# Kernel tuning notes

Measured on AMD Instinct MI355X. Metric: run time of the kernel, lower is better.

The kernel has to match this reference:

```python
import jax, jax.numpy as jnp
import numpy as np

EMBED_DIM = 1024
NUM_HEADS = 16
HEAD_DIM = EMBED_DIM // NUM_HEADS


def setup_inputs() -> dict:
    key = jax.random.key(0)
    ks = jax.random.split(key, 9)
    s = 1.0 / np.sqrt(EMBED_DIM)
    x = jax.random.normal(ks[0], (2, 2048, EMBED_DIM), dtype=jnp.float32)
    # nn.Linear weights are [out, in]; store transposed [in, out] for x @ W
    Wq = jax.random.uniform(ks[1], (EMBED_DIM, EMBED_DIM), jnp.float32, -s, s)
    bq = jax.random.uniform(ks[2], (EMBED_DIM,), jnp.float32, -s, s)
    Wk = jax.random.uniform(ks[3], (EMBED_DIM, EMBED_DIM), jnp.float32, -s, s)
    bk = jax.random.uniform(ks[4], (EMBED_DIM,), jnp.float32, -s, s)
    Wv = jax.random.uniform(ks[5], (EMBED_DIM, EMBED_DIM), jnp.float32, -s, s)
    bv = jax.random.uniform(ks[6], (EMBED_DIM,), jnp.float32, -s, s)
    Wo = jax.random.uniform(ks[7], (EMBED_DIM, EMBED_DIM), jnp.float32, -s, s)
    bo = jax.random.uniform(ks[8], (EMBED_DIM,), jnp.float32, -s, s)
    return {"x": x, "Wq": Wq, "bq": bq, "Wk": Wk, "bk": bk,
            "Wv": Wv, "bv": bv, "Wo": Wo, "bo": bo}


def reference(x, Wq, bq, Wk, bk, Wv, bv, Wo, bo):
    B, N, C = x.shape
    H, D = NUM_HEADS, HEAD_DIM
    scale = 1.0 / np.sqrt(D).astype(np.float32)
    # project and split heads: [B, H, N, D]
    q = (x @ Wq + bq).reshape(B, N, H, D).transpose(0, 2, 1, 3)
    k = (x @ Wk + bk).reshape(B, N, H, D).transpose(0, 2, 1, 3)
    v = (x @ Wv + bv).reshape(B, N, H, D).transpose(0, 2, 1, 3)
    scores = jnp.einsum('bhnd,bhmd->bhnm', q, k) * scale  # [B,H,N,N]
    probs = jax.nn.softmax(scores, axis=-1)
    attn = jnp.einsum('bhnm,bhmd->bhnd', probs, v)  # [B,H,N,D]
    attn = attn.transpose(0, 2, 1, 3).reshape(B, N, C)
    return attn @ Wo + bo
```

## Files before the change

### kernel.cpp

```cpp
#include <hip/hip_runtime.h>
#include <hip/hip_bf16.h>
#include <stdint.h>


#define DEVI __device__ __forceinline__

typedef __attribute__((ext_vector_type(8))) short bf16x8;
typedef __attribute__((ext_vector_type(4))) float f32x4;
typedef __attribute__((ext_vector_type(16))) float f32x16;

#define Z16 ((f32x16){0.f,0.f,0.f,0.f,0.f,0.f,0.f,0.f,0.f,0.f,0.f,0.f,0.f,0.f,0.f,0.f})

DEVI unsigned short f2bf(float f) {
  union { float f; uint32_t u; } v; v.f = f;
  uint32_t u = v.u;
  u += 0x7FFFu + ((u >> 16) & 1u);
  return (unsigned short)(u >> 16);
}

DEVI uint32_t cvtpk_bf16(float lo, float hi) {
  uint32_t r;
  asm("v_cvt_pk_bf16_f32 %0, %1, %2" : "=v"(r) : "v"(lo), "v"(hi));
  return r;
}

DEVI void pl32swap(uint32_t& a, uint32_t& b) {
  asm volatile("v_permlane32_swap_b32 %0, %1" : "+v"(a), "+v"(b));
}

DEVI float fexp2(float x) {
#if __has_builtin(__builtin_amdgcn_exp2f)
  return __builtin_amdgcn_exp2f(x);
#else
  return exp2f(x);
#endif
}

typedef __attribute__((address_space(3))) uint32_t lds_u32_t;
typedef const __attribute__((address_space(1))) uint32_t glb_u32_t;

DEVI void gl2lds16(const void* g, void* l) {
  __builtin_amdgcn_global_load_lds((glb_u32_t*)g, (lds_u32_t*)l, 16, 0, 0);
}

#define MFMA16(a, b, c) __builtin_amdgcn_mfma_f32_16x16x32_bf16((a), (b), (c), 0, 0, 0)
#define MFMA3216(a, b, c) __builtin_amdgcn_mfma_f32_32x32x16_bf16((a), (b), (c), 0, 0, 0)

__global__ void cvt_bf16_k(const float* __restrict__ in, unsigned short* __restrict__ out, int n8) {
  int i = blockIdx.x * blockDim.x + threadIdx.x;
  if (i >= n8) return;
  float4 a = ((const float4*)in)[i * 2];
  float4 b = ((const float4*)in)[i * 2 + 1];
  union { unsigned short s[8]; uint4 v; } u;
  u.s[0] = f2bf(a.x); u.s[1] = f2bf(a.y); u.s[2] = f2bf(a.z); u.s[3] = f2bf(a.w);
  u.s[4] = f2bf(b.x); u.s[5] = f2bf(b.y); u.s[6] = f2bf(b.z); u.s[7] = f2bf(b.w);
  ((uint4*)out)[i] = u.v;
}

__global__ void transpose_cvt4(const float* __restrict__ w0, const float* __restrict__ w1,
                               const float* __restrict__ w2, const float* __restrict__ w3,
                               unsigned short* __restrict__ o0, unsigned short* __restrict__ o1,
                               unsigned short* __restrict__ o2, unsigned short* __restrict__ o3) {
  const float* in = (blockIdx.z == 0) ? w0 : (blockIdx.z == 1) ? w1 : (blockIdx.z == 2) ? w2 : w3;
  unsigned short* out = (blockIdx.z == 0) ? o0 : (blockIdx.z == 1) ? o1 : (blockIdx.z == 2) ? o2 : o3;
  __shared__ float tile[32][33];
  int bx = blockIdx.x * 32, by = blockIdx.y * 32;
  int tx = threadIdx.x & 31, ty = threadIdx.x >> 5;
#pragma unroll
  for (int i = 0; i < 32; i += 8)
    tile[ty + i][tx] = in[(size_t)(by + ty + i) * 1024 + bx + tx];
  __syncthreads();
#pragma unroll
  for (int i = 0; i < 32; i += 8)
    out[(size_t)(bx + ty + i) * 1024 + by + tx] = f2bf(tile[tx][ty + i]);
}

__global__ __launch_bounds__(256, 2)
void gemm_qkv(const unsigned short* __restrict__ A, const unsigned short* __restrict__ Bt,
              const float* __restrict__ bq, const float* __restrict__ bk,
              const float* __restrict__ bv,
              unsigned short* __restrict__ Qb, unsigned short* __restrict__ Kb,
              unsigned short* __restrict__ Vtb) {
  __shared__ unsigned short lA[2][128 * 32];
  __shared__ unsigned short lB[2][128 * 32];
  const int t = threadIdx.x;
  const int mbase = blockIdx.y * 128, nbase = blockIdx.x * 128;
  const int wv = t >> 6, lane = t & 63, lr = lane & 15, lg = lane >> 4;
  const int wr = wv >> 1, wc = wv & 1;
  const int K = 1024;
  const int c0 = t, c1 = t + 256;

#define GSTAGE(buf, k0)                                                                     \
  do {                                                                                      \
    gl2lds16(A + ((size_t)(mbase + (c0 >> 2)) * K + (k0) + (c0 & 3) * 8), &lA[buf][c0 * 8]);\
    gl2lds16(Bt + ((size_t)(nbase + (c0 >> 2)) * K + (k0) + (c0 & 3) * 8), &lB[buf][c0 * 8]);\
    gl2lds16(A + ((size_t)(mbase + (c1 >> 2)) * K + (k0) + (c1 & 3) * 8), &lA[buf][c1 * 8]);\
    gl2lds16(Bt + ((size_t)(nbase + (c1 >> 2)) * K + (k0) + (c1 & 3) * 8), &lB[buf][c1 * 8]);\
  } while (0)

  f32x4 acc[4][4];
#pragma unroll
  for (int i = 0; i < 4; i++)
#pragma unroll
    for (int j = 0; j < 4; j++) acc[i][j] = (f32x4){0.f, 0.f, 0.f, 0.f};

  GSTAGE(0, 0);
  int buf = 0;
  for (int kk = 0; kk < 32; ++kk) {
    if (kk < 31) {
      GSTAGE(buf ^ 1, (kk + 1) * 32);
      asm volatile("s_waitcnt vmcnt(4)");
    } else {
      asm volatile("s_waitcnt vmcnt(0)");
    }
    __builtin_amdgcn_s_barrier();
    __builtin_amdgcn_sched_barrier(0);
    bf16x8 af[4], bfr[4];
#pragma unroll
    for (int i = 0; i < 4; i++)
      af[i] = *(const bf16x8*)&lA[buf][(wr * 64 + i * 16 + lr) * 32 + lg * 8];
#pragma unroll
    for (int j = 0; j < 4; j++)
      bfr[j] = *(const bf16x8*)&lB[buf][(wc * 64 + j * 16 + lr) * 32 + lg * 8];
    __builtin_amdgcn_s_setprio(1);
#pragma unroll
    for (int i = 0; i < 4; i++)
#pragma unroll
      for (int j = 0; j < 4; j++)
        acc[i][j] = MFMA16(af[i], bfr[j], acc[i][j]);
    __builtin_amdgcn_s_setprio(0);
    __builtin_amdgcn_s_barrier();
    buf ^= 1;
  }
#undef GSTAGE

#pragma unroll
  for (int i = 0; i < 4; i++) {
#pragma unroll
    for (int j = 0; j < 4; j++) {
#pragma unroll
      for (int r = 0; r < 4; r++) {
        int grow = mbase + wr * 64 + i * 16 + lg * 4 + r;
        int gcol = nbase + wc * 64 + j * 16 + lr;
        float v = acc[i][j][r];
        if (gcol < 1024) {
          Qb[(size_t)grow * 1024 + gcol] = f2bf((v + bq[gcol]) * 0.18033688011f);
        } else if (gcol < 2048) {
          int c2 = gcol - 1024;
          Kb[(size_t)grow * 1024 + c2] = f2bf(v + bk[c2]);
        } else {
          int vc = gcol - 2048, hh = vc >> 6, d = vc & 63;
          int bb = grow >> 11, np = grow & 2047;
          Vtb[((size_t)((bb * 16 + hh) * 64 + d) << 11) + np] = f2bf(v + bv[vc]);
        }
      }
    }
  }
}

__global__ __launch_bounds__(256, 2)
void gemm_out(const unsigned short* __restrict__ A, const unsigned short* __restrict__ Bt,
              const float* __restrict__ bias, float* __restrict__ outp) {
  __shared__ unsigned short lA[2][128 * 32];
  __shared__ unsigned short lB[2][128 * 32];
  const int t = threadIdx.x;
  const int mbase = blockIdx.y * 128, nbase = blockIdx.x * 128;
  const int wv = t >> 6, lane = t & 63, lr = lane & 15, lg = lane >> 4;
  const int wr = wv >> 1, wc = wv & 1;
  const int K = 1024, N = 1024;
  const int c0 = t, c1 = t + 256;

#define GSTAGE(buf, k0)                                                                     \
  do {                                                                                      \
    gl2lds16(A + ((size_t)(mbase + (c0 >> 2)) * K + (k0) + (c0 & 3) * 8), &lA[buf][c0 * 8]);\
    gl2lds16(Bt + ((size_t)(nbase + (c0 >> 2)) * K + (k0) + (c0 & 3) * 8), &lB[buf][c0 * 8]);\
    gl2lds16(A + ((size_t)(mbase + (c1 >> 2)) * K + (k0) + (c1 & 3) * 8), &lA[buf][c1 * 8]);\
    gl2lds16(Bt + ((size_t)(nbase + (c1 >> 2)) * K + (k0) + (c1 & 3) * 8), &lB[buf][c1 * 8]);\
  } while (0)

  f32x4 acc[4][4];
#pragma unroll
  for (int i = 0; i < 4; i++)
#pragma unroll
    for (int j = 0; j < 4; j++) acc[i][j] = (f32x4){0.f, 0.f, 0.f, 0.f};

  GSTAGE(0, 0);
  int buf = 0;
  for (int kk = 0; kk < 32; ++kk) {
    if (kk < 31) {
      GSTAGE(buf ^ 1, (kk + 1) * 32);
      asm volatile("s_waitcnt vmcnt(4)");
    } else {
      asm volatile("s_waitcnt vmcnt(0)");
    }
    __builtin_amdgcn_s_barrier();
    __builtin_amdgcn_sched_barrier(0);
    bf16x8 af[4], bfr[4];
#pragma unroll
    for (int i = 0; i < 4; i++)
      af[i] = *(const bf16x8*)&lA[buf][(wr * 64 + i * 16 + lr) * 32 + lg * 8];
#pragma unroll
    for (int j = 0; j < 4; j++)
      bfr[j] = *(const bf16x8*)&lB[buf][(wc * 64 + j * 16 + lr) * 32 + lg * 8];
    __builtin_amdgcn_s_setprio(1);
#pragma unroll
    for (int i = 0; i < 4; i++)
#pragma unroll
      for (int j = 0; j < 4; j++)
        acc[i][j] = MFMA16(af[i], bfr[j], acc[i][j]);
    __builtin_amdgcn_s_setprio(0);
    __builtin_amdgcn_s_barrier();
    buf ^= 1;
  }
#undef GSTAGE

#pragma unroll
  for (int i = 0; i < 4; i++)
#pragma unroll
    for (int j = 0; j < 4; j++)
#pragma unroll
      for (int r = 0; r < 4; r++) {
        int grow = mbase + wr * 64 + i * 16 + lg * 4 + r;
        int gcol = nbase + wc * 64 + j * 16 + lr;
        outp[(size_t)grow * N + gcol] = acc[i][j][r] + bias[gcol];
      }
}

__global__ __launch_bounds__(256, 2)
void attn_fwd(const unsigned short* __restrict__ Qb, const unsigned short* __restrict__ Kb,
              const unsigned short* __restrict__ Vtb, unsigned short* __restrict__ Ob) {
  const int hb = blockIdx.x, qt = blockIdx.y;
  const int h = hb & 15, b = hb >> 4;
  __shared__ unsigned short lK[2][128 * 64];
  __shared__ unsigned short lV[2][64 * 128];
  const int t = threadIdx.x, wv = t >> 6, lane = t & 63;
  const int q5 = lane & 31, hi = lane >> 5;
  const int sw7 = q5 & 7;
  const int sw15 = q5 & 15;

  const int qrow = b * 2048 + qt * 128 + wv * 32 + q5;
  const size_t qoff = (size_t)qrow * 1024 + h * 64;
  bf16x8 qf[4];
#pragma unroll
  for (int c = 0; c < 4; c++) qf[c] = *(const bf16x8*)&Qb[qoff + c * 16 + hi * 8];

  f32x16 o0 = Z16, o1 = Z16;
  float sum = 0.f;

  const size_t kbase = ((size_t)(b * 2048)) * 1024 + h * 64;
  const size_t vbase = ((size_t)((b * 16 + h) * 64)) * 2048;

#define STAGE(buf, kt)                                                                      \
  do {                                                                                      \
    _Pragma("unroll")                                                                       \
    for (int i = 0; i < 4; i++) {                                                           \
      int c = t + i * 256;                                                                  \
      int rk = c >> 3, sk = ((c & 7) ^ (rk & 7)) * 8;                                       \
      gl2lds16(Kb + kbase + (size_t)((kt) * 128 + rk) * 1024 + sk, &lK[buf][c * 8]);        \
      int rv = c >> 4, sv = ((c & 15) ^ (rv & 15)) * 8;                                     \
      gl2lds16(Vtb + vbase + (size_t)rv * 2048 + (kt) * 128 + sv, &lV[buf][c * 8]);         \
    }                                                                                       \
  } while (0)

  STAGE(0, 0);
  int cur = 0;

  for (int kt = 0; kt < 16; ++kt) {
    if (kt < 15) {
      STAGE(cur ^ 1, kt + 1);
      asm volatile("s_waitcnt vmcnt(8)");
    } else {
      asm volatile("s_waitcnt vmcnt(0)");
    }
    __builtin_amdgcn_s_barrier();
    __builtin_amdgcn_sched_barrier(0);

    const unsigned short* Kc = &lK[cur][0];
    f32x16 s[4];
#pragma unroll
    for (int i = 0; i < 4; i++) s[i] = Z16;
    __builtin_amdgcn_s_setprio(1);
#pragma unroll
    for (int ch = 0; ch < 4; ch++) {
      const int g = ((ch * 2 + hi) ^ sw7) * 8;
#pragma unroll
      for (int sub = 0; sub < 4; sub++) {
        bf16x8 kf = *(const bf16x8*)&Kc[(sub * 32 + q5) * 64 + g];
        s[sub] = MFMA3216(kf, qf[ch], s[sub]);
      }
    }
    __builtin_amdgcn_s_setprio(0);

    float su0 = 0.f, su1 = 0.f, su2 = 0.f, su3 = 0.f;
#pragma unroll
    for (int i = 0; i < 4; i++) {
#pragma unroll
      for (int r = 0; r < 16; r += 4) {
        s[i][r + 0] = fexp2(s[i][r + 0]); su0 += s[i][r + 0];
        s[i][r + 1] = fexp2(s[i][r + 1]); su1 += s[i][r + 1];
        s[i][r + 2] = fexp2(s[i][r + 2]); su2 += s[i][r + 2];
        s[i][r + 3] = fexp2(s[i][r + 3]); su3 += s[i][r + 3];
      }
    }
    {
      float su = (su0 + su1) + (su2 + su3);
      uint32_t sa = __float_as_uint(su), sb = sa;
      pl32swap(sa, sb);
      sum += __uint_as_float(sa) + __uint_as_float(sb);
    }

    const unsigned short* Vc = &lV[cur][0];
#pragma unroll
    for (int g2 = 0; g2 < 2; g2++) {
#pragma unroll
      for (int c16 = 0; c16 < 4; c16++) {
        const int base = 8 * (c16 & 1);
        const int ti = 2 * g2 + (c16 >> 1);
        uint32_t u0 = cvtpk_bf16(s[ti][base + 0], s[ti][base + 1]);
        uint32_t u1 = cvtpk_bf16(s[ti][base + 2], s[ti][base + 3]);
        uint32_t u2 = cvtpk_bf16(s[ti][base + 4], s[ti][base + 5]);
        uint32_t u3 = cvtpk_bf16(s[ti][base + 6], s[ti][base + 7]);
        pl32swap(u0, u2);
        pl32swap(u1, u3);
        union { uint32_t u[4]; bf16x8 v; } f;
        f.u[0] = u0; f.u[1] = u1; f.u[2] = u2; f.u[3] = u3;
        const int e = (((g2 * 8 + c16 * 2 + hi)) ^ sw15) * 8;
        bf16x8 v0 = *(const bf16x8*)&Vc[q5 * 128 + e];
        bf16x8 v1 = *(const bf16x8*)&Vc[(32 + q5) * 128 + e];
        __builtin_amdgcn_s_setprio(1);
        o0 = MFMA3216(v0, f.v, o0);
        o1 = MFMA3216(v1, f.v, o1);
        __builtin_amdgcn_s_setprio(0);
      }
    }
    __builtin_amdgcn_s_barrier();
    cur ^= 1;
  }
#undef STAGE

  float inv = 1.0f / sum;
  const size_t ob = (size_t)qrow * 1024 + h * 64;
#pragma unroll
  for (int a = 0; a < 4; a++) {
    uint2 pk0, pk1;
    pk0.x = cvtpk_bf16(o0[4 * a + 0] * inv, o0[4 * a + 1] * inv);
    pk0.y = cvtpk_bf16(o0[4 * a + 2] * inv, o0[4 * a + 3] * inv);
    *(uint2*)&Ob[ob + 8 * a + 4 * hi] = pk0;
    pk1.x = cvtpk_bf16(o1[4 * a + 0] * inv, o1[4 * a + 1] * inv);
    pk1.y = cvtpk_bf16(o1[4 * a + 2] * inv, o1[4 * a + 3] * inv);
    *(uint2*)&Ob[ob + 32 + 8 * a + 4 * hi] = pk1;
  }
}

extern "C" void kernel_launch(void* const* d_in, const int* in_sizes, int n_in,
                              void* d_out, int out_size, void* d_ws, size_t ws_size,
                              hipStream_t stream) {
  const float* x  = (const float*)d_in[0];
  const float* Wq = (const float*)d_in[1];
  const float* bq = (const float*)d_in[2];
  const float* Wk = (const float*)d_in[3];
  const float* bk = (const float*)d_in[4];
  const float* Wv = (const float*)d_in[5];
  const float* bv = (const float*)d_in[6];
  const float* Wo = (const float*)d_in[7];
  const float* bo = (const float*)d_in[8];
  float* out = (float*)d_out;

  char* ws = (char*)d_ws;
  const size_t MB = 1024u * 1024u;
  unsigned short* xb    = (unsigned short*)(ws + 0);
  unsigned short* wqkvt = (unsigned short*)(ws + 8 * MB);
  unsigned short* wot   = (unsigned short*)(ws + 14 * MB);
  unsigned short* Qb    = (unsigned short*)(ws + 16 * MB);
  unsigned short* Kb    = (unsigned short*)(ws + 24 * MB);
  unsigned short* Vtb   = (unsigned short*)(ws + 32 * MB);
  unsigned short* Ab    = (unsigned short*)(ws + 40 * MB);

  cvt_bf16_k<<<2048, 256, 0, stream>>>(x, xb, 524288);
  transpose_cvt4<<<dim3(32, 32, 4), 256, 0, stream>>>(
      Wq, Wk, Wv, Wo, wqkvt, wqkvt + 1024 * 1024, wqkvt + 2048 * 1024, wot);
  gemm_qkv<<<dim3(24, 32), 256, 0, stream>>>(xb, wqkvt, bq, bk, bv, Qb, Kb, Vtb);
  attn_fwd<<<dim3(32, 16), 256, 0, stream>>>(Qb, Kb, Vtb, Ab);
  gemm_out<<<dim3(8, 32), 256, 0, stream>>>(Ab, wot, bo, out);
}
```

Baseline: 125.1 us.

## Restructure QKV GEMM to 256x256 tiles with 8 waves and swizzled LDS

Rewrites the QKV projection GEMM to use 256x256 output tiles per 512-thread block (8 waves, each computing 128x64), with a K-step of 64 split into two halves. Global-to-LDS loads are interleaved with MFMA phases, LDS rows are XOR-swizzled, and block indices are remapped for L2 locality. The aim is higher arithmetic intensity, fewer LDS bank conflicts and better overlap of loads with compute. The cost is more registers per thread and a grid of only 192 blocks, which may underfill the GPU's compute units.

Result: slower. 154.2 us (+23.2%).

```diff
diff --git a/kernel.cpp b/kernel.cpp
--- a/kernel.cpp
+++ b/kernel.cpp
@@ -75,77 +75,149 @@
     out[(size_t)(bx + ty + i) * 1024 + by + tx] = f2bf(tile[tx][ty + i]);
 }
 
-__global__ __launch_bounds__(256, 2)
+template <int NH>
+DEVI void ph_mfma(f32x4 (&acc)[8][4], const bf16x8 (&af)[8], bf16x8 b0, bf16x8 b1) {
+#pragma unroll
+  for (int mf = 0; mf < 8; mf++) {
+    acc[mf][NH * 2 + 0] = MFMA16(af[mf], b0, acc[mf][NH * 2 + 0]);
+    acc[mf][NH * 2 + 1] = MFMA16(af[mf], b1, acc[mf][NH * 2 + 1]);
+  }
+}
+
+__global__ __launch_bounds__(512, 2)
 void gemm_qkv(const unsigned short* __restrict__ A, const unsigned short* __restrict__ Bt,
               const float* __restrict__ bq, const float* __restrict__ bk,
               const float* __restrict__ bv,
               unsigned short* __restrict__ Qb, unsigned short* __restrict__ Kb,
               unsigned short* __restrict__ Vtb) {
-  __shared__ unsigned short lA[2][128 * 32];
-  __shared__ unsigned short lB[2][128 * 32];
+  __shared__ unsigned short lA[2][2][256 * 32];
+  __shared__ unsigned short lB[2][2][256 * 32];
   const int t = threadIdx.x;
-  const int mbase = blockIdx.y * 128, nbase = blockIdx.x * 128;
-  const int wv = t >> 6, lane = t & 63, lr = lane & 15, lg = lane >> 4;
-  const int wr = wv >> 1, wc = wv & 1;
-  const int K = 1024;
-  const int c0 = t, c1 = t + 256;
-
-#define GSTAGE(buf, k0)                                                                     \
-  do {                                                                                      \
-    gl2lds16(A + ((size_t)(mbase + (c0 >> 2)) * K + (k0) + (c0 & 3) * 8), &lA[buf][c0 * 8]);\
-    gl2lds16(Bt + ((size_t)(nbase + (c0 >> 2)) * K + (k0) + (c0 & 3) * 8), &lB[buf][c0 * 8]);\
-    gl2lds16(A + ((size_t)(mbase + (c1 >> 2)) * K + (k0) + (c1 & 3) * 8), &lA[buf][c1 * 8]);\
-    gl2lds16(Bt + ((size_t)(nbase + (c1 >> 2)) * K + (k0) + (c1 & 3) * 8), &lB[buf][c1 * 8]);\
+  const int wid = t >> 6, lane = t & 63, lr = lane & 15, lg = lane >> 4;
+  const int wr = wid >> 2, wc = wid & 3;
+  const int swz = ((blockIdx.x & 7) * 24) + (blockIdx.x >> 3);
+  const int by = swz / 12, bx = swz % 12;
+  const int mbase = by * 256, nbase = bx * 256;
+  const int sw2 = (lr ^ (lr >> 2)) & 3;
+
+  const int G0 = wid * 128 + lane, G1 = G0 + 64;
+  const int r0 = G0 >> 2, k0 = ((G0 & 3) ^ ((r0 ^ (r0 >> 2)) & 3)) * 8;
+  const int r1 = G1 >> 2, k1 = ((G1 & 3) ^ ((r1 ^ (r1 >> 2)) & 3)) * 8;
+
+#define STG_A(bf, kh, kt) do { \
+    gl2lds16(A + (size_t)(mbase + r0) * 1024 + (kt) * 64 + (kh) * 32 + k0, &lA[bf][kh][G0 * 8]); \
+    gl2lds16(A + (size_t)(mbase + r1) * 1024 + (kt) * 64 + (kh) * 32 + k1, &lA[bf][kh][G1 * 8]); \
   } while (0)
-
-  f32x4 acc[4][4];
-#pragma unroll
-  for (int i = 0; i < 4; i++)
+#define STG_B(bf, kh, kt) do { \
+    gl2lds16(Bt + (size_t)(nbase + r0) * 1024 + (kt) * 64 + (kh) * 32 + k0, &lB[bf][kh][G0 * 8]); \
+    gl2lds16(Bt + (size_t)(nbase + r1) * 1024 + (kt) * 64 + (kh) * 32 + k1, &lB[bf][kh][G1 * 8]); \
+  } while (0)
+
+  f32x4 acc[8][4];
+#pragma unroll
+  for (int i = 0; i < 8; i++)
 #pragma unroll
     for (int j = 0; j < 4; j++) acc[i][j] = (f32x4){0.f, 0.f, 0.f, 0.f};
-
-  GSTAGE(0, 0);
-  int buf = 0;
-  for (int kk = 0; kk < 32; ++kk) {
-    if (kk < 31) {
-      GSTAGE(buf ^ 1, (kk + 1) * 32);
-      asm volatile("s_waitcnt vmcnt(4)");
-    } else {
-      asm volatile("s_waitcnt vmcnt(0)");
-    }
-    __builtin_amdgcn_s_barrier();
-    __builtin_amdgcn_sched_barrier(0);
-    bf16x8 af[4], bfr[4];
-#pragma unroll
-    for (int i = 0; i < 4; i++)
-      af[i] = *(const bf16x8*)&lA[buf][(wr * 64 + i * 16 + lr) * 32 + lg * 8];
-#pragma unroll
-    for (int j = 0; j < 4; j++)
-      bfr[j] = *(const bf16x8*)&lB[buf][(wc * 64 + j * 16 + lr) * 32 + lg * 8];
-    __builtin_amdgcn_s_setprio(1);
-#pragma unroll
-    for (int i = 0; i < 4; i++)
-#pragma unroll
-      for (int j = 0; j < 4; j++)
-        acc[i][j] = MFMA16(af[i], bfr[j], acc[i][j]);
-    __builtin_amdgcn_s_setprio(0);
-    __builtin_amdgcn_s_barrier();
-    buf ^= 1;
-  }
-#undef GSTAGE
-
-#pragma unroll
-  for (int i = 0; i < 4; i++) {
+  bf16x8 af[8];
+
+  STG_A(0, 0, 0); STG_B(0, 0, 0); STG_A(0, 1, 0); STG_B(0, 1, 0);
+  asm volatile("s_waitcnt vmcnt(4)");
+  __builtin_amdgcn_s_barrier();
+  __builtin_amdgcn_sched_barrier(0);
+
+  const int aoff = (wr * 128 + lr) * 32 + (lg ^ sw2) * 8;
+  const int boff = (wc * 64 + lr) * 32 + (lg ^ sw2) * 8;
+
+  for (int kt = 0; kt < 16; ++kt) {
+    const int bf = kt & 1, nb = bf ^ 1;
+    const bool pf = (kt < 15);
+    {
+      const unsigned short* Ah = &lA[bf][0][0];
+      const unsigned short* Bh = &lB[bf][0][0];
+#pragma unroll
+      for (int mf = 0; mf < 8; mf++) af[mf] = *(const bf16x8*)&Ah[aoff + mf * 512];
+      bf16x8 b0 = *(const bf16x8*)&Bh[boff + 0];
+      bf16x8 b1 = *(const bf16x8*)&Bh[boff + 512];
+      if (pf) STG_A(nb, 0, kt + 1);
+      __builtin_amdgcn_s_barrier();
+      asm volatile("s_waitcnt lgkmcnt(0)");
+      __builtin_amdgcn_sched_barrier(0);
+      __builtin_amdgcn_s_setprio(1);
+      ph_mfma<0>(acc, af, b0, b1);
+      __builtin_amdgcn_s_setprio(0);
+      __builtin_amdgcn_s_barrier();
+      __builtin_amdgcn_sched_barrier(0);
+    }
+    {
+      const unsigned short* Bh = &lB[bf][0][0];
+      bf16x8 b0 = *(const bf16x8*)&Bh[boff + 1024];
+      bf16x8 b1 = *(const bf16x8*)&Bh[boff + 1536];
+      if (pf) {
+        STG_B(nb, 0, kt + 1);
+        asm volatile("s_waitcnt vmcnt(4)");
+      } else {
+        asm volatile("s_waitcnt vmcnt(0)");
+      }
+      __builtin_amdgcn_s_barrier();
+      asm volatile("s_waitcnt lgkmcnt(0)");
+      __builtin_amdgcn_sched_barrier(0);
+      __builtin_amdgcn_s_setprio(1);
+      ph_mfma<1>(acc, af, b0, b1);
+      __builtin_amdgcn_s_setprio(0);
+      __builtin_amdgcn_s_barrier();
+      __builtin_amdgcn_sched_barrier(0);
+    }
+    {
+      const unsigned short* Ah = &lA[bf][1][0];
+      const unsigned short* Bh = &lB[bf][1][0];
+#pragma unroll
+      for (int mf = 0; mf < 8; mf++) af[mf] = *(const bf16x8*)&Ah[aoff + mf * 512];
+      bf16x8 b0 = *(const bf16x8*)&Bh[boff + 0];
+      bf16x8 b1 = *(const bf16x8*)&Bh[boff + 512];
+      if (pf) STG_A(nb, 1, kt + 1);
+      __builtin_amdgcn_s_barrier();
+      asm volatile("s_waitcnt lgkmcnt(0)");
+      __builtin_amdgcn_sched_barrier(0);
+      __builtin_amdgcn_s_setprio(1);
+      ph_mfma<0>(acc, af, b0, b1);
+      __builtin_amdgcn_s_setprio(0);
+      __builtin_amdgcn_s_barrier();
+      __builtin_amdgcn_sched_barrier(0);
+    }
+    {
+      const unsigned short* Bh = &lB[bf][1][0];
+      bf16x8 b0 = *(const bf16x8*)&Bh[boff + 1024];
+      bf16x8 b1 = *(const bf16x8*)&Bh[boff + 1536];
+      if (pf) {
+        STG_B(nb, 1, kt + 1);
+        asm volatile("s_waitcnt vmcnt(4)");
+      }
+      __builtin_amdgcn_s_barrier();
+      asm volatile("s_waitcnt lgkmcnt(0)");
+      __builtin_amdgcn_sched_barrier(0);
+      __builtin_amdgcn_s_setprio(1);
+      ph_mfma<1>(acc, af, b0, b1);
+      __builtin_amdgcn_s_setprio(0);
+      __builtin_amdgcn_s_barrier();
+      __builtin_amdgcn_sched_barrier(0);
+    }
+  }
+#undef STG_A
+#undef STG_B
+
+  const int region = bx >> 2;
+#pragma unroll
+  for (int i = 0; i < 8; i++) {
 #pragma unroll
     for (int j = 0; j < 4; j++) {
 #pragma unroll
       for (int r = 0; r < 4; r++) {
-        int grow = mbase + wr * 64 + i * 16 + lg * 4 + r;
+        int grow = mbase + wr * 128 + i * 16 + lg * 4 + r;
         int gcol = nbase + wc * 64 + j * 16 + lr;
         float v = acc[i][j][r];
-        if (gcol < 1024) {
+        if (region == 0) {
           Qb[(size_t)grow * 1024 + gcol] = f2bf((v + bq[gcol]) * 0.18033688011f);
-        } else if (gcol < 2048) {
+        } else if (region == 1) {
           int c2 = gcol - 1024;
           Kb[(size_t)grow * 1024 + c2] = f2bf(v + bk[c2]);
         } else {
@@ -379,7 +451,7 @@
   cvt_bf16_k<<<2048, 256, 0, stream>>>(x, xb, 524288);
   transpose_cvt4<<<dim3(32, 32, 4), 256, 0, stream>>>(
       Wq, Wk, Wv, Wo, wqkvt, wqkvt + 1024 * 1024, wqkvt + 2048 * 1024, wot);
-  gemm_qkv<<<dim3(24, 32), 256, 0, stream>>>(xb, wqkvt, bq, bk, bv, Qb, Kb, Vtb);
+  gemm_qkv<<<192, 512, 0, stream>>>(xb, wqkvt, bq, bk, bv, Qb, Kb, Vtb);
   attn_fwd<<<dim3(32, 16), 256, 0, stream>>>(Qb, Kb, Vtb, Ab);
   gemm_out<<<dim3(8, 32), 256, 0, stream>>>(Ab, wot, bo, out);
 }
```
